# Performance work log

Measured on AMD Instinct MI355X. Metric: run time of the kernel, lower is better.

## Reference

```python
import jax, jax.numpy as jnp
import numpy as np

B, S, H, L = 256, 128, 1024, 2
FEATS = {"t": 300, "v": 35, "a": 74}


def setup_inputs() -> dict:
    key = jax.random.key(0)
    inp = {}
    k = 0

    def nk():
        nonlocal k
        k += 1
        return jax.random.fold_in(key, k)

    inp["t_input"] = jax.random.normal(nk(), (B, S, FEATS["t"]), jnp.float32)
    inp["v_input"] = jax.random.normal(nk(), (B, S, FEATS["v"]), jnp.float32)
    inp["a_input"] = jax.random.normal(nk(), (B, S, FEATS["a"]), jnp.float32)
    std = 1.0 / np.sqrt(H)
    for m, f in FEATS.items():
        in_sizes = [f + 2 * H, H]  # layer0 gets modality feat + two cross-modal hiddens
        for l in range(L):
            inp[f"Wih_{m}{l}"] = jax.random.normal(nk(), (4 * H, in_sizes[l]), jnp.float32) * std
            inp[f"Whh_{m}{l}"] = jax.random.normal(nk(), (4 * H, H), jnp.float32) * std
            inp[f"bih_{m}{l}"] = jax.random.normal(nk(), (4 * H,), jnp.float32) * std
            inp[f"bhh_{m}{l}"] = jax.random.normal(nk(), (4 * H,), jnp.float32) * std
    inp["Wd"] = jax.random.normal(nk(), (1, 3 * H), jnp.float32) * np.sqrt(2.0 / (1 + 3 * H))
    inp["bd"] = jnp.zeros((1,), jnp.float32)
    return inp


def _cell(x, h, c, Wih, Whh, bih, bhh):
    # PyTorch LSTM gate order: i, f, g, o
    z = x @ Wih.T + h @ Whh.T + bih + bhh  # [B, 4H]
    i, f, g, o = jnp.split(z, 4, axis=-1)
    c_new = jax.nn.sigmoid(f) * c + jax.nn.sigmoid(i) * jnp.tanh(g)
    h_new = jax.nn.sigmoid(o) * jnp.tanh(c_new)
    return h_new, c_new


def _stack_cell(x, hs, cs, layers):
    new_h, new_c = [], []
    inp = x
    for l, (Wih, Whh, bih, bhh) in enumerate(layers):
        h, c = _cell(inp, hs[l], cs[l], Wih, Whh, bih, bhh)
        new_h.append(h)
        new_c.append(c)
        inp = h
    return jnp.stack(new_h), jnp.stack(new_c)


def _forward(t_input, v_input, a_input, pt, pv, pa, Wd, bd):
    z = jnp.zeros((L, B, H), t_input.dtype)
    carry0 = (z, z, z, z, z, z)
    xs = (t_input.transpose(1, 0, 2), v_input.transpose(1, 0, 2), a_input.transpose(1, 0, 2))

    def step(carry, x):
        ht, ct, hv, cv, ha, ca = carry
        xt, xv, xa = x
        tf, vf, af = ht[-1], hv[-1], ha[-1]  # top-layer hiddens from previous step
        t_in = jnp.concatenate([xt, vf, af], axis=-1)
        v_in = jnp.concatenate([xv, tf, af], axis=-1)
        a_in = jnp.concatenate([xa, tf, vf], axis=-1)
        ht, ct = _stack_cell(t_in, ht, ct, pt)
        hv, cv = _stack_cell(v_in, hv, cv, pv)
        ha, ca = _stack_cell(a_in, ha, ca, pa)
        return (ht, ct, hv, cv, ha, ca), None

    (ht, ct, hv, cv, ha, ca), _ = jax.lax.scan(step, carry0, xs)
    feat = jnp.concatenate([ht[-1], hv[-1], ha[-1]], axis=-1)  # [B, 3H]
    return feat @ Wd.T + bd  # [B, 1]


def reference(t_input, v_input, a_input,
              Wih_t0, Whh_t0, bih_t0, bhh_t0, Wih_t1, Whh_t1, bih_t1, bhh_t1,
              Wih_v0, Whh_v0, bih_v0, bhh_v0, Wih_v1, Whh_v1, bih_v1, bhh_v1,
              Wih_a0, Whh_a0, bih_a0, bhh_a0, Wih_a1, Whh_a1, bih_a1, bhh_a1,
              Wd, bd):
    pt = [(Wih_t0, Whh_t0, bih_t0, bhh_t0), (Wih_t1, Whh_t1, bih_t1, bhh_t1)]
    pv = [(Wih_v0, Whh_v0, bih_v0, bhh_v0), (Wih_v1, Whh_v1, bih_v1, bhh_v1)]
    pa = [(Wih_a0, Whh_a0, bih_a0, bhh_a0), (Wih_a1, Whh_a1, bih_a1, bhh_a1)]
    return _forward(t_input, v_input, a_input, pt, pv, pa, Wd, bd)
```

## Files before the change

kernel.cpp:

```cpp
#include <hip/hip_runtime.h>
#include <hip/hip_fp16.h>
#include <cstdint>
#include <cstddef>


typedef _Float16 half8 __attribute__((ext_vector_type(8)));
typedef float floatx4 __attribute__((ext_vector_type(4)));

__device__ __forceinline__ void gload16(const void* g, void* l) {
  __builtin_amdgcn_global_load_lds(
      (const __attribute__((address_space(1))) void*)g,
      (__attribute__((address_space(3))) void*)l, 16, 0, 0);
}

__device__ __forceinline__ float fsig(float x) {
  return 1.f / (1.f + __expf(-x));
}
__device__ __forceinline__ float ftanhf(float x) {
  x = fminf(15.f, fmaxf(-15.f, x));
  float e = __expf(2.f * x);
  return (e - 1.f) / (e + 1.f);
}

struct ModParam {
  const __half* xseg; int Kx;
  const __half* inseg; int Kin;
  const __half* W;
  const float* bias;
  float* c;
  __half* dst0; int ds0, off0;
  __half* dst1; int ds1, off1;
  __half* dst2; int ds2, off2;
  __half* feat; int featoff;
};
struct PhaseParams { ModParam m[3]; };

__global__ __launch_bounds__(256, 3) void lstm_phase(PhaseParams P) {
  const int b_ = blockIdx.x;
  const int xcd = b_ & 7, rnd = b_ >> 3;
  const int pairIdx = xcd * 24 + (rnd >> 2);
  const int mtile = rnd & 3;
  const int mod = pairIdx >> 6;
  const int bn = pairIdx & 63;
  const ModParam p = P.m[mod];
  const int Ktot = p.Kx + p.Kin;
  const int tid = threadIdx.x;
  const int lane = tid & 63, wid = tid >> 6;
  const int ln = lane & 15, lm = lane >> 4, c4 = lane & 3;
  const int wr = wid >> 1, wc = wid & 1;

  __shared__ __align__(16) __half As[64][64];
  __shared__ __align__(16) __half Bs[64][64];

  floatx4 acc[2][2];
#pragma unroll
  for (int mi = 0; mi < 2; ++mi)
#pragma unroll
    for (int ni = 0; ni < 2; ++ni) acc[mi][ni] = (floatx4)0.f;

  const int nK = Ktot >> 6;
  for (int ks = 0; ks < nK; ++ks) {
    const int k0 = ks << 6;
    const __half* abase;
    int astr;
    if (k0 < p.Kx) { abase = p.xseg + k0; astr = p.Kx; }
    else           { abase = p.inseg + (k0 - p.Kx); astr = p.Kin; }
#pragma unroll
    for (int it = 0; it < 2; ++it) {
      int idx = it * 256 + tid;
      int row = idx >> 3, pc = idx & 7;
      int lc = pc ^ (row & 7);
      gload16(abase + (size_t)(mtile * 64 + row) * astr + lc * 8,
              ((__half*)As) + (size_t)idx * 8);
    }
    const __half* bbase = p.W + (size_t)(bn * 64) * Ktot + k0;
#pragma unroll
    for (int it = 0; it < 2; ++it) {
      int idx = it * 256 + tid;
      int row = idx >> 3, pc = idx & 7;
      int lc = pc ^ (row & 7);
      gload16(bbase + (size_t)row * Ktot + lc * 8,
              ((__half*)Bs) + (size_t)idx * 8);
    }
    __syncthreads();
#pragma unroll
    for (int kh = 0; kh < 2; ++kh) {
      half8 av[2], bv[2];
#pragma unroll
      for (int mi = 0; mi < 2; ++mi) {
        int row = wr * 32 + mi * 16 + ln;
        int ch = (kh * 4 + lm) ^ (row & 7);
        av[mi] = *(const half8*)&As[row][ch * 8];
      }
#pragma unroll
      for (int ni = 0; ni < 2; ++ni) {
        int row = wc * 32 + ni * 16 + ln;
        int ch = (kh * 4 + lm) ^ (row & 7);
        bv[ni] = *(const half8*)&Bs[row][ch * 8];
      }
#pragma unroll
      for (int mi = 0; mi < 2; ++mi)
#pragma unroll
        for (int ni = 0; ni < 2; ++ni)
          acc[mi][ni] = __builtin_amdgcn_mfma_f32_16x16x32_f16(
              av[mi], bv[ni], acc[mi][ni], 0, 0, 0);
    }
    __syncthreads();
  }

#pragma unroll
  for (int ni = 0; ni < 2; ++ni) {
    const int ncol = bn * 64 + wc * 32 + ni * 16 + ln;
    const float bia = p.bias[ncol];
    const int j = ncol >> 2;
#pragma unroll
    for (int mi = 0; mi < 2; ++mi) {
#pragma unroll
      for (int r = 0; r < 4; ++r) {
        float v = acc[mi][ni][r] + bia;
        float g1 = __shfl_xor(v, 1);
        float g2 = __shfl_xor(v, 2);
        float g3 = __shfl_xor(v, 3);
        int m0 = c4 ^ 0, m1 = c4 ^ 1, m2 = c4 ^ 2, m3 = c4 ^ 3;
        float zi = m0 == 0 ? v : (m0 == 1 ? g1 : (m0 == 2 ? g2 : g3));
        float zf = m1 == 0 ? v : (m1 == 1 ? g1 : (m1 == 2 ? g2 : g3));
        float zg = m2 == 0 ? v : (m2 == 1 ? g1 : (m2 == 2 ? g2 : g3));
        float zo = m3 == 0 ? v : (m3 == 1 ? g1 : (m3 == 2 ? g2 : g3));
        const int b = mtile * 64 + wr * 32 + mi * 16 + lm * 4 + r;
        float cp = p.c[b * 1024 + j];
        float cn = fsig(zf) * cp + fsig(zi) * ftanhf(zg);
        float hn = fsig(zo) * ftanhf(cn);
        __half h16 = __float2half(hn);
        if (c4 == 0) {
          if (p.dst0) p.dst0[(size_t)b * p.ds0 + p.off0 + j] = h16;
        } else if (c4 == 1) {
          if (p.dst1) p.dst1[(size_t)b * p.ds1 + p.off1 + j] = h16;
        } else if (c4 == 2) {
          if (p.dst2) p.dst2[(size_t)b * p.ds2 + p.off2 + j] = h16;
        } else {
          p.c[b * 1024 + j] = cn;
          if (p.feat) p.feat[(size_t)b * 3072 + p.featoff + j] = h16;
        }
      }
    }
  }
}

__global__ void pack_w(__half* dst, const float* Wih, const float* Whh,
                       float* bdst, const float* bih, const float* bhh,
                       int f, int fpad, int hih, int Ktot) {
  long long i = (long long)blockIdx.x * 256 + threadIdx.x;
  long long tot = (long long)4096 * Ktot;
  if (i < tot) {
    int n = (int)(i / Ktot), k = (int)(i % Ktot);
    int nsrc = (n & 3) * 1024 + (n >> 2);
    float v;
    if (k < fpad)
      v = (k < f) ? Wih[(size_t)nsrc * (f + hih) + k] : 0.f;
    else if (k < fpad + hih)
      v = Wih[(size_t)nsrc * (f + hih) + f + (k - fpad)];
    else
      v = Whh[(size_t)nsrc * 1024 + (k - fpad - hih)];
    dst[i] = __float2half(v);
  }
  if (i < 4096) {
    int nsrc = ((int)i & 3) * 1024 + ((int)i >> 2);
    bdst[i] = bih[nsrc] + bhh[nsrc];
  }
}

__global__ void pack_x(__half* dst, const float* x, int f, int fpad) {
  long long i = (long long)blockIdx.x * 256 + threadIdx.x;
  long long tot = (long long)128 * 256 * fpad;
  if (i >= tot) return;
  int k = (int)(i % fpad);
  long long r = i / fpad;
  int b = (int)(r % 256);
  int t = (int)(r / 256);
  dst[i] = (k < f) ? __float2half(x[((size_t)b * 128 + t) * f + k])
                   : __float2half(0.f);
}

__global__ void final_dot(const __half* feat, const float* Wd, const float* bd,
                          float* out) {
  int b = blockIdx.x, tid = threadIdx.x;
  float s = 0.f;
  for (int j = tid; j < 3072; j += 256)
    s += __half2float(feat[(size_t)b * 3072 + j]) * Wd[j];
  __shared__ float red[256];
  red[tid] = s;
  __syncthreads();
  for (int o = 128; o > 0; o >>= 1) {
    if (tid < o) red[tid] += red[tid + o];
    __syncthreads();
  }
  if (tid == 0) out[b] = red[0] + bd[0];
}

extern "C" void kernel_launch(void* const* d_in, const int* in_sizes, int n_in,
                              void* d_out, int out_size, void* d_ws, size_t ws_size,
                              hipStream_t stream) {
  const int B = 256, S = 128, H = 1024, NG = 4096;
  const int FRAW[3] = {300, 35, 74};
  const int FPAD[3] = {320, 64, 128};

  const float* xin[3] = {(const float*)d_in[0], (const float*)d_in[1],
                         (const float*)d_in[2]};
  const float *Wih0[3], *Whh0[3], *bih0[3], *bhh0[3];
  const float *Wih1[3], *Whh1[3], *bih1[3], *bhh1[3];
  for (int m = 0; m < 3; ++m) {
    int bidx = 3 + m * 8;
    Wih0[m] = (const float*)d_in[bidx + 0];
    Whh0[m] = (const float*)d_in[bidx + 1];
    bih0[m] = (const float*)d_in[bidx + 2];
    bhh0[m] = (const float*)d_in[bidx + 3];
    Wih1[m] = (const float*)d_in[bidx + 4];
    Whh1[m] = (const float*)d_in[bidx + 5];
    bih1[m] = (const float*)d_in[bidx + 6];
    bhh1[m] = (const float*)d_in[bidx + 7];
  }
  const float* Wd = (const float*)d_in[27];
  const float* bd = (const float*)d_in[28];

  uint8_t* wsb = (uint8_t*)d_ws;
  size_t off = 0;
  auto alloc = [&](size_t bytes) -> void* {
    void* p = wsb + off;
    off += (bytes + 255) & ~(size_t)255;
    return p;
  };

  __half* W0[3];
  __half* W1[3];
  int K0[3];
  for (int m = 0; m < 3; ++m) {
    K0[m] = FPAD[m] + 3 * H;
    W0[m] = (__half*)alloc((size_t)NG * K0[m] * 2);
  }
  for (int m = 0; m < 3; ++m) W1[m] = (__half*)alloc((size_t)NG * 2 * H * 2);
  float* biasB = (float*)alloc((size_t)6 * NG * 4);
  __half* X16[3];
  for (int m = 0; m < 3; ++m)
    X16[m] = (__half*)alloc((size_t)S * B * FPAD[m] * 2);
  size_t stateStart = off;
  __half* In0[3];
  __half* In1[3];
  for (int m = 0; m < 3; ++m) In0[m] = (__half*)alloc((size_t)2 * B * 3072 * 2);
  for (int m = 0; m < 3; ++m) In1[m] = (__half*)alloc((size_t)2 * B * 2048 * 2);
  float* cbuf = (float*)alloc((size_t)6 * B * H * 4);
  size_t stateEnd = off;
  __half* featB = (__half*)alloc((size_t)B * 3072 * 2);

  if (off > ws_size) return;

  for (int m = 0; m < 3; ++m) {
    long long tot0 = (long long)NG * K0[m];
    pack_w<<<dim3((unsigned)((tot0 + 255) / 256)), 256, 0, stream>>>(
        W0[m], Wih0[m], Whh0[m], biasB + m * NG, bih0[m], bhh0[m],
        FRAW[m], FPAD[m], 2 * H, K0[m]);
    long long tot1 = (long long)NG * 2 * H;
    pack_w<<<dim3((unsigned)((tot1 + 255) / 256)), 256, 0, stream>>>(
        W1[m], Wih1[m], Whh1[m], biasB + (3 + m) * NG, bih1[m], bhh1[m],
        0, 0, H, 2 * H);
    long long totx = (long long)S * B * FPAD[m];
    pack_x<<<dim3((unsigned)((totx + 255) / 256)), 256, 0, stream>>>(
        X16[m], xin[m], FRAW[m], FPAD[m]);
  }
  hipMemsetAsync(wsb + stateStart, 0, stateEnd - stateStart, stream);

  for (int t = 0; t < S; ++t) {
    int pq = t & 1;
    __half* in0cur[3], *in0nxt[3], *in1cur[3], *in1nxt[3];
    for (int m = 0; m < 3; ++m) {
      in0cur[m] = In0[m] + (size_t)pq * B * 3072;
      in0nxt[m] = In0[m] + (size_t)(pq ^ 1) * B * 3072;
      in1cur[m] = In1[m] + (size_t)pq * B * 2048;
      in1nxt[m] = In1[m] + (size_t)(pq ^ 1) * B * 2048;
    }

    PhaseParams PA;
    for (int m = 0; m < 3; ++m) {
      ModParam& q = PA.m[m];
      q.xseg = X16[m] + (size_t)t * B * FPAD[m];
      q.Kx = FPAD[m];
      q.inseg = in0cur[m];
      q.Kin = 3072;
      q.W = W0[m];
      q.bias = biasB + m * NG;
      q.c = cbuf + (size_t)m * B * H;
      q.dst0 = in1cur[m]; q.ds0 = 2048; q.off0 = 0;
      q.dst1 = in0nxt[m]; q.ds1 = 3072; q.off1 = 2048;
      q.dst2 = nullptr;   q.ds2 = 0;    q.off2 = 0;
      q.feat = nullptr;   q.featoff = 0;
    }
    lstm_phase<<<dim3(768), 256, 0, stream>>>(PA);

    PhaseParams PB;
    for (int m = 0; m < 3; ++m) {
      ModParam& q = PB.m[m];
      q.xseg = nullptr; q.Kx = 0;
      q.inseg = in1cur[m]; q.Kin = 2048;
      q.W = W1[m];
      q.bias = biasB + (3 + m) * NG;
      q.c = cbuf + (size_t)(3 + m) * B * H;
      q.feat = (t == S - 1) ? featB : nullptr;
      q.featoff = m * H;
      q.ds0 = 3072; q.ds1 = 3072; q.ds2 = 2048;
      if (m == 0) {
        q.dst0 = in0nxt[1]; q.off0 = 0;
        q.dst1 = in0nxt[2]; q.off1 = 0;
        q.dst2 = in1nxt[0]; q.off2 = 1024;
      } else if (m == 1) {
        q.dst0 = in0nxt[0]; q.off0 = 0;
        q.dst1 = in0nxt[2]; q.off1 = 1024;
        q.dst2 = in1nxt[1]; q.off2 = 1024;
      } else {
        q.dst0 = in0nxt[0]; q.off0 = 1024;
        q.dst1 = in0nxt[1]; q.off1 = 1024;
        q.dst2 = in1nxt[2]; q.off2 = 1024;
      }
    }
    lstm_phase<<<dim3(768), 256, 0, stream>>>(PB);
  }

  final_dot<<<dim3(256), 256, 0, stream>>>(featB, Wd, bd, (float*)d_out);
}
```

Measured before the change: 10.82 ms.

## Pre-tile weights and activations into K-chunk blocks and add 5-stage LDS pipeline

Weights and activation buffers are repacked so that each 64x64 K-tile is a contiguous 8 KB block, laid out k-chunk-major with batch rows contiguous. That lets global-to-LDS loads be fully contiguous and replaces the XOR-swizzled row-major tiles. The GEMM loop becomes a 5-slot ring of LDS buffers that prefetches 3 tiles ahead, using explicit vmcnt waits and a single barrier per iteration instead of two syncthreads. The cost is a larger LDS footprint (80 KB), with launch bounds lowered from 3 to 2 blocks per CU. Correctness depends on the hand-written vmcnt counts matching the issued loads.

```diff
diff --git a/kernel.cpp b/kernel.cpp
--- a/kernel.cpp
+++ b/kernel.cpp
@@ -12,7 +12,6 @@
       (const __attribute__((address_space(1))) void*)g,
       (__attribute__((address_space(3))) void*)l, 16, 0, 0);
 }
-
 __device__ __forceinline__ float fsig(float x) {
   return 1.f / (1.f + __expf(-x));
 }
@@ -23,81 +22,74 @@
 }
 
 struct ModParam {
-  const __half* xseg; int Kx;
-  const __half* inseg; int Kin;
+  const __half* xseg;
+  const __half* inseg;
   const __half* W;
   const float* bias;
   float* c;
-  __half* dst0; int ds0, off0;
-  __half* dst1; int ds1, off1;
-  __half* dst2; int ds2, off2;
+  __half* dst0; __half* dst1; __half* dst2;
+  int off0, off1, off2;
   __half* feat; int featoff;
+  int Kx, Kin;
 };
 struct PhaseParams { ModParam m[3]; };
 
-__global__ __launch_bounds__(256, 3) void lstm_phase(PhaseParams P) {
+__global__ __launch_bounds__(256, 2) void lstm_phase(PhaseParams P) {
   const int b_ = blockIdx.x;
   const int xcd = b_ & 7, rnd = b_ >> 3;
   const int pairIdx = xcd * 24 + (rnd >> 2);
-  const int mtile = rnd & 3;
+  const int mt = rnd & 3;
   const int mod = pairIdx >> 6;
-  const int bn = pairIdx & 63;
+  const int nt = pairIdx & 63;
   const ModParam p = P.m[mod];
-  const int Ktot = p.Kx + p.Kin;
+  const int nKt = (p.Kx + p.Kin) >> 6;
+  const int KxT = p.Kx >> 6;
   const int tid = threadIdx.x;
   const int lane = tid & 63, wid = tid >> 6;
+  const int wr = wid >> 1, wc = wid & 1;
   const int ln = lane & 15, lm = lane >> 4, c4 = lane & 3;
-  const int wr = wid >> 1, wc = wid & 1;
-
-  __shared__ __align__(16) __half As[64][64];
-  __shared__ __align__(16) __half Bs[64][64];
+
+  __shared__ __align__(16) __half lds[5 * 8192];
 
   floatx4 acc[2][2];
 #pragma unroll
-  for (int mi = 0; mi < 2; ++mi)
-#pragma unroll
-    for (int ni = 0; ni < 2; ++ni) acc[mi][ni] = (floatx4)0.f;
-
-  const int nK = Ktot >> 6;
-  for (int ks = 0; ks < nK; ++ks) {
-    const int k0 = ks << 6;
+  for (int a = 0; a < 2; ++a)
+#pragma unroll
+    for (int b = 0; b < 2; ++b) acc[a][b] = (floatx4)0.f;
+
+  auto stage = [&](int kt, int slot) {
     const __half* abase;
-    int astr;
-    if (k0 < p.Kx) { abase = p.xseg + k0; astr = p.Kx; }
-    else           { abase = p.inseg + (k0 - p.Kx); astr = p.Kin; }
-#pragma unroll
-    for (int it = 0; it < 2; ++it) {
-      int idx = it * 256 + tid;
-      int row = idx >> 3, pc = idx & 7;
-      int lc = pc ^ (row & 7);
-      gload16(abase + (size_t)(mtile * 64 + row) * astr + lc * 8,
-              ((__half*)As) + (size_t)idx * 8);
-    }
-    const __half* bbase = p.W + (size_t)(bn * 64) * Ktot + k0;
-#pragma unroll
-    for (int it = 0; it < 2; ++it) {
-      int idx = it * 256 + tid;
-      int row = idx >> 3, pc = idx & 7;
-      int lc = pc ^ (row & 7);
-      gload16(bbase + (size_t)row * Ktot + lc * 8,
-              ((__half*)Bs) + (size_t)idx * 8);
-    }
-    __syncthreads();
-#pragma unroll
-    for (int kh = 0; kh < 2; ++kh) {
+    int kq0;
+    if (kt < KxT) { abase = p.xseg;  kq0 = kt * 8; }
+    else          { abase = p.inseg; kq0 = (kt - KxT) * 8; }
+#pragma unroll
+    for (int o = 0; o < 2; ++o) {
+      int idx = o * 256 + tid;
+      int kql = idx >> 6, row = idx & 63;
+      gload16(abase + ((size_t)(kq0 + kql) * 256 + mt * 64 + row) * 8,
+              &lds[slot * 8192 + idx * 8]);
+    }
+    const __half* wb = p.W + (size_t)(nt * nKt + kt) * 4096;
+#pragma unroll
+    for (int o = 0; o < 2; ++o) {
+      int idx = o * 256 + tid;
+      gload16(wb + (size_t)idx * 8, &lds[slot * 8192 + 4096 + idx * 8]);
+    }
+  };
+
+  auto compute = [&](int slot) {
+    const __half* base = &lds[slot * 8192];
+#pragma unroll
+    for (int ks = 0; ks < 2; ++ks) {
       half8 av[2], bv[2];
 #pragma unroll
-      for (int mi = 0; mi < 2; ++mi) {
-        int row = wr * 32 + mi * 16 + ln;
-        int ch = (kh * 4 + lm) ^ (row & 7);
-        av[mi] = *(const half8*)&As[row][ch * 8];
-      }
-#pragma unroll
-      for (int ni = 0; ni < 2; ++ni) {
-        int row = wc * 32 + ni * 16 + ln;
-        int ch = (kh * 4 + lm) ^ (row & 7);
-        bv[ni] = *(const half8*)&Bs[row][ch * 8];
-      }
+      for (int mi = 0; mi < 2; ++mi)
+        av[mi] = *(const half8*)&base[((ks * 4 + lm) * 64 + wr * 32 +
+                                       mi * 16 + ln) * 8];
+#pragma unroll
+      for (int ni = 0; ni < 2; ++ni)
+        bv[ni] = *(const half8*)&base[4096 + ((ks * 4 + lm) * 64 + wc * 32 +
+                                              ni * 16 + ln) * 8];
 #pragma unroll
       for (int mi = 0; mi < 2; ++mi)
 #pragma unroll
@@ -105,12 +97,37 @@
           acc[mi][ni] = __builtin_amdgcn_mfma_f32_16x16x32_f16(
               av[mi], bv[ni], acc[mi][ni], 0, 0, 0);
     }
-    __syncthreads();
-  }
-
+  };
+
+  stage(0, 0);
+  stage(1, 1);
+  stage(2, 2);
+  int sc = 0, sp = 3;
+  for (int kt = 0; kt < nKt; ++kt) {
+    if (kt + 3 < nKt) {
+      stage(kt + 3, sp);
+      asm volatile("s_waitcnt vmcnt(12)" ::: "memory");
+    } else if (kt + 2 < nKt) {
+      asm volatile("s_waitcnt vmcnt(8)" ::: "memory");
+    } else if (kt + 1 < nKt) {
+      asm volatile("s_waitcnt vmcnt(4)" ::: "memory");
+    } else {
+      asm volatile("s_waitcnt vmcnt(0)" ::: "memory");
+    }
+    __builtin_amdgcn_s_barrier();
+    __builtin_amdgcn_sched_barrier(0);
+    compute(sc);
+    sc = (sc == 4) ? 0 : sc + 1;
+    sp = (sp == 4) ? 0 : sp + 1;
+  }
+
+  auto wrH = [&](__half* d, int off, int br, int j, __half v) {
+    int col = off + j;
+    d[(size_t)(col >> 3) * 2048 + br * 8 + (col & 7)] = v;
+  };
 #pragma unroll
   for (int ni = 0; ni < 2; ++ni) {
-    const int ncol = bn * 64 + wc * 32 + ni * 16 + ln;
+    const int ncol = nt * 64 + wc * 32 + ni * 16 + ln;
     const float bia = p.bias[ncol];
     const int j = ncol >> 2;
 #pragma unroll
@@ -121,25 +138,25 @@
         float g1 = __shfl_xor(v, 1);
         float g2 = __shfl_xor(v, 2);
         float g3 = __shfl_xor(v, 3);
-        int m0 = c4 ^ 0, m1 = c4 ^ 1, m2 = c4 ^ 2, m3 = c4 ^ 3;
+        int m0 = c4, m1 = c4 ^ 1, m2 = c4 ^ 2, m3 = c4 ^ 3;
         float zi = m0 == 0 ? v : (m0 == 1 ? g1 : (m0 == 2 ? g2 : g3));
         float zf = m1 == 0 ? v : (m1 == 1 ? g1 : (m1 == 2 ? g2 : g3));
         float zg = m2 == 0 ? v : (m2 == 1 ? g1 : (m2 == 2 ? g2 : g3));
         float zo = m3 == 0 ? v : (m3 == 1 ? g1 : (m3 == 2 ? g2 : g3));
-        const int b = mtile * 64 + wr * 32 + mi * 16 + lm * 4 + r;
-        float cp = p.c[b * 1024 + j];
+        const int br = mt * 64 + wr * 32 + mi * 16 + lm * 4 + r;
+        float cp = p.c[br * 1024 + j];
         float cn = fsig(zf) * cp + fsig(zi) * ftanhf(zg);
         float hn = fsig(zo) * ftanhf(cn);
         __half h16 = __float2half(hn);
         if (c4 == 0) {
-          if (p.dst0) p.dst0[(size_t)b * p.ds0 + p.off0 + j] = h16;
+          if (p.dst0) wrH(p.dst0, p.off0, br, j, h16);
         } else if (c4 == 1) {
-          if (p.dst1) p.dst1[(size_t)b * p.ds1 + p.off1 + j] = h16;
+          if (p.dst1) wrH(p.dst1, p.off1, br, j, h16);
         } else if (c4 == 2) {
-          if (p.dst2) p.dst2[(size_t)b * p.ds2 + p.off2 + j] = h16;
+          if (p.dst2) wrH(p.dst2, p.off2, br, j, h16);
         } else {
-          p.c[b * 1024 + j] = cn;
-          if (p.feat) p.feat[(size_t)b * 3072 + p.featoff + j] = h16;
+          p.c[br * 1024 + j] = cn;
+          if (p.feat) p.feat[(size_t)br * 3072 + p.featoff + j] = h16;
         }
       }
     }
@@ -151,9 +168,16 @@
                        int f, int fpad, int hih, int Ktot) {
   long long i = (long long)blockIdx.x * 256 + threadIdx.x;
   long long tot = (long long)4096 * Ktot;
+  const int nKt = Ktot >> 6;
   if (i < tot) {
-    int n = (int)(i / Ktot), k = (int)(i % Ktot);
+    int e = (int)(i & 7);
+    int col = (int)((i >> 3) & 63);
+    int kql = (int)((i >> 9) & 7);
+    long long r2 = i >> 12;
+    int kt = (int)(r2 % nKt), nt = (int)(r2 / nKt);
+    int n = nt * 64 + col;
     int nsrc = (n & 3) * 1024 + (n >> 2);
+    int k = kt * 64 + kql * 8 + e;
     float v;
     if (k < fpad)
       v = (k < f) ? Wih[(size_t)nsrc * (f + hih) + k] : 0.f;
@@ -173,10 +197,14 @@
   long long i = (long long)blockIdx.x * 256 + threadIdx.x;
   long long tot = (long long)128 * 256 * fpad;
   if (i >= tot) return;
-  int k = (int)(i % fpad);
-  long long r = i / fpad;
-  int b = (int)(r % 256);
-  int t = (int)(r / 256);
+  int e = (int)(i & 7);
+  long long u = i >> 3;
+  int b = (int)(u & 255);
+  long long v = u >> 8;
+  int nq = fpad >> 3;
+  int kq = (int)(v % nq);
+  int t = (int)(v / nq);
+  int k = kq * 8 + e;
   dst[i] = (k < f) ? __float2half(x[((size_t)b * 128 + t) * f + k])
                    : __float2half(0.f);
 }
@@ -288,9 +316,9 @@
       q.W = W0[m];
       q.bias = biasB + m * NG;
       q.c = cbuf + (size_t)m * B * H;
-      q.dst0 = in1cur[m]; q.ds0 = 2048; q.off0 = 0;
-      q.dst1 = in0nxt[m]; q.ds1 = 3072; q.off1 = 2048;
-      q.dst2 = nullptr;   q.ds2 = 0;    q.off2 = 0;
+      q.dst0 = in1cur[m]; q.off0 = 0;
+      q.dst1 = in0nxt[m]; q.off1 = 2048;
+      q.dst2 = nullptr;   q.off2 = 0;
       q.feat = nullptr;   q.featoff = 0;
     }
     lstm_phase<<<dim3(768), 256, 0, stream>>>(PA);
@@ -305,7 +333,6 @@
       q.c = cbuf + (size_t)(3 + m) * B * H;
       q.feat = (t == S - 1) ? featB : nullptr;
       q.featoff = m * H;
-      q.ds0 = 3072; q.ds1 = 3072; q.ds2 = 2048;
       if (m == 0) {
         q.dst0 = in0nxt[1]; q.off0 = 0;
         q.dst1 = in0nxt[2]; q.off1 = 0;
```

New measurement: 12.45 ms. +15.0%, slower.
